# Performance work log

Hardware: AMD Instinct MI355X
Metric: run time of the kernel (lower is better)

## Reference

```python
import jax, jax.numpy as jnp
import numpy as np

NUM_ENTS = 100000
NUM_RELS2 = 1000  # num_rels * 2
H_DIM = 128
NUM_EDGES = 2000000
RRELU_SLOPE = (1.0 / 8.0 + 1.0 / 3.0) / 2.0  # F.rrelu eval-mode negative slope


def l2_normalize(x, eps=1e-12):
    # F.normalize along last dim
    n = jnp.sqrt(jnp.sum(x * x, axis=-1, keepdims=True))
    return x / jnp.maximum(n, eps)


def setup_inputs() -> dict:
    key = jax.random.key(0)
    ks = jax.random.split(key, 11)
    s = 1.0 / np.sqrt(H_DIM)
    return {
        "ent_emb": jax.random.normal(ks[0], (NUM_ENTS, H_DIM), jnp.float32),
        "rel_emb": jax.random.normal(ks[1], (NUM_RELS2, H_DIM), jnp.float32) * s,
        "his": jax.random.normal(ks[2], (NUM_ENTS, H_DIM), jnp.float32),
        "W_neighbor": jax.random.normal(ks[3], (H_DIM, H_DIM), jnp.float32) * s,
        "W_self": jax.random.normal(ks[4], (H_DIM, H_DIM), jnp.float32) * s,
        "time_gate_weight": jax.random.normal(ks[5], (H_DIM, H_DIM), jnp.float32) * s,
        "time_gate_bias": jnp.zeros((H_DIM,), jnp.float32),
        "edge_norm": jax.random.uniform(ks[6], (NUM_EDGES,), jnp.float32),
        "src": jax.random.randint(ks[7], (NUM_EDGES,), 0, NUM_ENTS, jnp.int32),
        "dst": jax.random.randint(ks[8], (NUM_EDGES,), 0, NUM_ENTS, jnp.int32),
        "etype": jax.random.randint(ks[9], (NUM_EDGES,), 0, NUM_RELS2, jnp.int32),
    }


def reference(ent_emb, rel_emb, his, W_neighbor, W_self, time_gate_weight,
              time_gate_bias, edge_norm, src, dst, etype):
    # layer_norm=True branch: L2-normalize entity embeddings (F.normalize)
    h = l2_normalize(ent_emb)                                   # [N, D]
    # UnionRGCNLayer message: (h[src] + rel_emb[etype]) @ W, scaled by edge norm
    node = h[src] + rel_emb[etype]                              # [E, D] gather
    msg = (node @ W_neighbor) * edge_norm[:, None]              # [E, D]
    agg = jax.ops.segment_sum(msg, dst, num_segments=NUM_ENTS)  # [N, D] scatter
    # self-loop + rrelu (eval mode: leaky with mean slope)
    h_cur = agg + h @ W_self
    h_cur = jnp.where(h_cur >= 0, h_cur, RRELU_SLOPE * h_cur)
    # time gate: blend current with historical embedding
    gate = jax.nn.sigmoid(h_cur @ time_gate_weight + time_gate_bias)
    out = gate * h_cur + (1.0 - gate) * his
    return out
```

## Files before the change

### kernel.cpp

```cpp
#include <hip/hip_runtime.h>
#include <math.h>

#define NUM_ENTS   100000
#define HD         128
#define NUM_EDGES  2000000
#define NUM_RELS2  1000
#define RRELU_SLOPE 0.22916666666666666f
#define NBLK 391
#define NPAD (NBLK * 256)
#define EQ4  (NUM_EDGES / 4)
#define EBLK ((EQ4 + 255) / 256)

#define SB_CNT 391
#define SB_HB  25000
#define SB_RB  125
#define SB_WP  24
#define SB_TOTAL (SB_CNT + SB_HB + SB_RB + SB_WP)

typedef __attribute__((ext_vector_type(8))) short bf16x8;
typedef __attribute__((ext_vector_type(4))) float f32x4;

__device__ __forceinline__ float bf2f(unsigned short h) {
    union { unsigned int u; float f; } v;
    v.u = ((unsigned int)h) << 16;
    return v.f;
}
__device__ __forceinline__ void unpack2(unsigned int u, float& lo, float& hi) {
    union { unsigned int u; float f; } a, b;
    a.u = u << 16;
    b.u = u & 0xffff0000u;
    lo = a.f; hi = b.f;
}
__device__ __forceinline__ unsigned short f2bf(float f) {
    union { float f; unsigned int u; } v; v.f = f;
    unsigned int r = 0x7fffu + ((v.u >> 16) & 1u);
    return (unsigned short)((v.u + r) >> 16);
}

__global__ void __launch_bounds__(256)
setup_kernel(const float* __restrict__ ent, const float* __restrict__ rel,
             const float* __restrict__ Wn, const float* __restrict__ Ws,
             const float* __restrict__ Wt,
             int* __restrict__ cnt, unsigned short* __restrict__ hb,
             unsigned short* __restrict__ rb, unsigned short* __restrict__ Wp) {
    const int bid = blockIdx.x, tid = threadIdx.x;
    if (bid < SB_CNT) {
        cnt[bid * 256 + tid] = 0;
    } else if (bid < SB_CNT + SB_HB) {
        const int row = (bid - SB_CNT) * 4 + (tid >> 6);
        const int lane = tid & 63;
        const float2 v = *(const float2*)(ent + (size_t)row * HD + lane * 2);
        float ss = v.x * v.x + v.y * v.y;
        #pragma unroll
        for (int m = 1; m < 64; m <<= 1) ss += __shfl_xor(ss, m, 64);
        const float inv = 1.0f / fmaxf(sqrtf(ss), 1e-12f);
        const unsigned int o = (unsigned int)f2bf(v.x * inv) |
                               ((unsigned int)f2bf(v.y * inv) << 16);
        *(unsigned int*)(hb + (size_t)row * HD + lane * 2) = o;
    } else if (bid < SB_CNT + SB_HB + SB_RB) {
        const int i = (bid - SB_CNT - SB_HB) * 256 + tid;
        const float4 v = ((const float4*)rel)[i];
        ushort4 o;
        o.x = f2bf(v.x); o.y = f2bf(v.y); o.z = f2bf(v.z); o.w = f2bf(v.w);
        ((ushort4*)rb)[i] = o;
    } else {
        const int blk = (bid - SB_CNT - SB_HB - SB_RB) * 4 + (tid >> 6);
        const int lane = tid & 63;
        const int w = blk >> 5, rem = blk & 31, t = rem >> 2, kt = rem & 3;
        const float* W = (w == 0) ? Wn : (w == 1) ? Ws : Wt;
        const int n  = t * 16 + (lane & 15);
        const int k0 = kt * 32 + (lane >> 4) * 8;
        unsigned short tmp[8];
        #pragma unroll
        for (int j = 0; j < 8; ++j) tmp[j] = f2bf(W[(size_t)(k0 + j) * HD + n]);
        unsigned short* d = Wp + ((size_t)blk * 64 + lane) * 8;
        *(ushort4*)(d + 0) = make_ushort4(tmp[0], tmp[1], tmp[2], tmp[3]);
        *(ushort4*)(d + 4) = make_ushort4(tmp[4], tmp[5], tmp[6], tmp[7]);
    }
}

__global__ void __launch_bounds__(256)
hist_kernel(const int* __restrict__ dst, int* __restrict__ cnt, int* __restrict__ pos) {
    const int i = blockIdx.x * 256 + threadIdx.x;
    if (i < EQ4) {
        const int4 d4 = ((const int4*)dst)[i];
        int4 p4;
        p4.x = atomicAdd(&cnt[d4.x], 1);
        p4.y = atomicAdd(&cnt[d4.y], 1);
        p4.z = atomicAdd(&cnt[d4.z], 1);
        p4.w = atomicAdd(&cnt[d4.w], 1);
        ((int4*)pos)[i] = p4;
    }
}

__global__ void __launch_bounds__(256)
scan1_kernel(const int* __restrict__ cnt, int* __restrict__ offs, int* __restrict__ bsum) {
    __shared__ int tmp[256];
    const int t = threadIdx.x;
    const int i = blockIdx.x * 256 + t;
    const int v = cnt[i];
    tmp[t] = v;
    __syncthreads();
    #pragma unroll
    for (int d = 1; d < 256; d <<= 1) {
        const int a = (t >= d) ? tmp[t - d] : 0;
        __syncthreads();
        tmp[t] += a;
        __syncthreads();
    }
    offs[i] = tmp[t] - v;
    if (t == 255) bsum[blockIdx.x] = tmp[255];
}

__global__ void __launch_bounds__(512)
scan2_kernel(int* __restrict__ bsum) {
    __shared__ int tmp[512];
    const int t = threadIdx.x;
    const int v = (t < NBLK) ? bsum[t] : 0;
    tmp[t] = v;
    __syncthreads();
    #pragma unroll
    for (int d = 1; d < 512; d <<= 1) {
        const int a = (t >= d) ? tmp[t - d] : 0;
        __syncthreads();
        tmp[t] += a;
        __syncthreads();
    }
    if (t < NBLK) bsum[t] = tmp[t] - v;
}

__global__ void __launch_bounds__(256)
scan3_kernel(int* __restrict__ offs, const int* __restrict__ bsum) {
    const int i = blockIdx.x * 256 + threadIdx.x;
    offs[i] += bsum[blockIdx.x];
}

__global__ void __launch_bounds__(256)
permute_kernel(const int* __restrict__ dst, const int* __restrict__ src,
               const int* __restrict__ ety, const float* __restrict__ enorm,
               const int* __restrict__ offs, const int* __restrict__ pos,
               uint2* __restrict__ recs) {
    const int i = blockIdx.x * 256 + threadIdx.x;
    if (i < EQ4) {
        const int4 d4 = ((const int4*)dst)[i];
        const int4 s4 = ((const int4*)src)[i];
        const int4 t4 = ((const int4*)ety)[i];
        const float4 n4 = ((const float4*)enorm)[i];
        const int4 p4 = ((const int4*)pos)[i];
        recs[offs[d4.x] + p4.x] = make_uint2((unsigned int)s4.x | ((unsigned int)t4.x << 17), __float_as_uint(n4.x));
        recs[offs[d4.y] + p4.y] = make_uint2((unsigned int)s4.y | ((unsigned int)t4.y << 17), __float_as_uint(n4.y));
        recs[offs[d4.z] + p4.z] = make_uint2((unsigned int)s4.z | ((unsigned int)t4.z << 17), __float_as_uint(n4.z));
        recs[offs[d4.w] + p4.w] = make_uint2((unsigned int)s4.w | ((unsigned int)t4.w << 17), __float_as_uint(n4.w));
    }
}

__device__ __forceinline__ void accum8(float* acc, uint4 hv, uint4 rv, float w) {
    float h0, h1, r0, r1;
    unpack2(hv.x, h0, h1); unpack2(rv.x, r0, r1);
    acc[0] += (h0 + r0) * w; acc[1] += (h1 + r1) * w;
    unpack2(hv.y, h0, h1); unpack2(rv.y, r0, r1);
    acc[2] += (h0 + r0) * w; acc[3] += (h1 + r1) * w;
    unpack2(hv.z, h0, h1); unpack2(rv.z, r0, r1);
    acc[4] += (h0 + r0) * w; acc[5] += (h1 + r1) * w;
    unpack2(hv.w, h0, h1); unpack2(rv.w, r0, r1);
    acc[6] += (h0 + r0) * w; acc[7] += (h1 + r1) * w;
}

__global__ void __launch_bounds__(256, 4)
gather_mfma(const unsigned short* __restrict__ hb,
            const unsigned short* __restrict__ rb,
            const int* __restrict__ offs,
            const uint2* __restrict__ recs,
            const unsigned short* __restrict__ Wp,
            const float* __restrict__ bias,
            const float* __restrict__ his,
            float* __restrict__ out) {
    __shared__ unsigned short tile[4][16 * 136];
    const int tid = threadIdx.x;
    const int wv = tid >> 6, lane = tid & 63;
    const int m0 = blockIdx.x * 64 + wv * 16;
    if (m0 >= NUM_ENTS) return;
    const int grp = lane >> 4, sub = lane & 15;
    const int rA = lane & 15, quad = lane >> 4;
    unsigned short* T = tile[wv];
    const unsigned short* hbp = hb + sub * 8;
    const unsigned short* rbp = rb + sub * 8;

    #pragma unroll
    for (int b = 0; b < 4; ++b) {
        const int rloc = b * 4 + grp;
        const int d = m0 + rloc;
        const int beg = offs[d], end = offs[d + 1];
        float acc[8] = {0.f, 0.f, 0.f, 0.f, 0.f, 0.f, 0.f, 0.f};
        int i = beg;
        uint2 rcA[4];
        #pragma unroll
        for (int k = 0; k < 4; ++k) rcA[k] = recs[min(i + k, NUM_EDGES - 1)];
        while (__any(i < end)) {
            uint2 rcB[4];
            #pragma unroll
            for (int k = 0; k < 4; ++k) rcB[k] = recs[min(i + 4 + k, NUM_EDGES - 1)];
            uint4 hv[4], rv[4]; float w[4];
            #pragma unroll
            for (int k = 0; k < 4; ++k) {
                w[k] = (i + k) < end ? __uint_as_float(rcA[k].y) : 0.f;
                hv[k] = *(const uint4*)(hbp + (size_t)(rcA[k].x & 0x1FFFFu) * HD);
                rv[k] = *(const uint4*)(rbp + (size_t)(rcA[k].x >> 17) * HD);
            }
            #pragma unroll
            for (int k = 0; k < 4; ++k) accum8(acc, hv[k], rv[k], w[k]);
            #pragma unroll
            for (int k = 0; k < 4; ++k) rcA[k] = rcB[k];
            i += 4;
        }
        unsigned short* dT = T + rloc * 136 + sub * 8;
        *(ushort4*)(dT + 0) = make_ushort4(f2bf(acc[0]), f2bf(acc[1]), f2bf(acc[2]), f2bf(acc[3]));
        *(ushort4*)(dT + 4) = make_ushort4(f2bf(acc[4]), f2bf(acc[5]), f2bf(acc[6]), f2bf(acc[7]));
    }

    const bf16x8* WF = (const bf16x8*)Wp;
    f32x4 acc1[8];
    #pragma unroll
    for (int t = 0; t < 8; ++t) acc1[t] = (f32x4)0.f;

    #pragma unroll
    for (int ph = 0; ph < 2; ++ph) {
        bf16x8 a[4];
        if (ph == 0) {
            #pragma unroll
            for (int kt = 0; kt < 4; ++kt)
                a[kt] = *(const bf16x8*)(T + rA * 136 + kt * 32 + quad * 8);
        } else {
            const unsigned short* base = hb + (size_t)(m0 + rA) * HD + quad * 8;
            #pragma unroll
            for (int kt = 0; kt < 4; ++kt)
                a[kt] = *(const bf16x8*)(base + kt * 32);
        }
        #pragma unroll
        for (int t = 0; t < 8; ++t) {
            #pragma unroll
            for (int kt = 0; kt < 4; ++kt) {
                const bf16x8 bfr = WF[(size_t)(ph * 32 + t * 4 + kt) * 64 + lane];
                acc1[t] = __builtin_amdgcn_mfma_f32_16x16x32_bf16(a[kt], bfr, acc1[t], 0, 0, 0);
            }
        }
    }

    #pragma unroll
    for (int t = 0; t < 8; ++t)
        #pragma unroll
        for (int r = 0; r < 4; ++r)
            acc1[t][r] = acc1[t][r] >= 0.f ? acc1[t][r] : RRELU_SLOPE * acc1[t][r];

    #pragma unroll
    for (int t = 0; t < 8; ++t)
        #pragma unroll
        for (int r = 0; r < 4; ++r)
            T[(quad * 4 + r) * 136 + t * 16 + rA] = f2bf(acc1[t][r]);

    bf16x8 a3[4];
    #pragma unroll
    for (int kt = 0; kt < 4; ++kt)
        a3[kt] = *(const bf16x8*)(T + rA * 136 + kt * 32 + quad * 8);

    #pragma unroll
    for (int t = 0; t < 8; ++t) {
        const float bn = bias[t * 16 + rA];
        f32x4 c2 = (f32x4){bn, bn, bn, bn};
        #pragma unroll
        for (int kt = 0; kt < 4; ++kt) {
            const bf16x8 bfr = WF[(size_t)(64 + t * 4 + kt) * 64 + lane];
            c2 = __builtin_amdgcn_mfma_f32_16x16x32_bf16(a3[kt], bfr, c2, 0, 0, 0);
        }
        const int col = t * 16 + rA;
        #pragma unroll
        for (int r = 0; r < 4; ++r) {
            const size_t row = (size_t)(m0 + quad * 4 + r);
            const float g = 1.f / (1.f + __expf(-c2[r]));
            const float h = his[row * HD + col];
            out[row * HD + col] = g * acc1[t][r] + (1.f - g) * h;
        }
    }
}

extern "C" void kernel_launch(void* const* d_in, const int* in_sizes, int n_in,
                              void* d_out, int out_size, void* d_ws, size_t ws_size,
                              hipStream_t stream) {
    const float* ent   = (const float*)d_in[0];
    const float* rel   = (const float*)d_in[1];
    const float* his   = (const float*)d_in[2];
    const float* Wn    = (const float*)d_in[3];
    const float* Ws    = (const float*)d_in[4];
    const float* Wt    = (const float*)d_in[5];
    const float* bias  = (const float*)d_in[6];
    const float* enorm = (const float*)d_in[7];
    const int* src = (const int*)d_in[8];
    const int* dst = (const int*)d_in[9];
    const int* ety = (const int*)d_in[10];
    float* out = (float*)d_out;

    char* p = (char*)d_ws;
    unsigned short* hb = (unsigned short*)p;  p += (size_t)NUM_ENTS * HD * 2;
    unsigned short* rb = (unsigned short*)p;  p += (size_t)NUM_RELS2 * HD * 2;
    unsigned short* Wp = (unsigned short*)p;  p += (size_t)96 * 64 * 8 * 2;
    int* cnt  = (int*)p;                      p += (size_t)NPAD * 4;
    int* offs = (int*)p;                      p += (size_t)NPAD * 4;
    int* bsum = (int*)p;                      p += 512 * 4;
    int* pos  = (int*)p;                      p += (size_t)NUM_EDGES * 4;
    uint2* recs = (uint2*)p;

    setup_kernel<<<SB_TOTAL, 256, 0, stream>>>(ent, rel, Wn, Ws, Wt, cnt, hb, rb, Wp);
    hist_kernel<<<EBLK, 256, 0, stream>>>(dst, cnt, pos);
    scan1_kernel<<<NBLK, 256, 0, stream>>>(cnt, offs, bsum);
    scan2_kernel<<<1, 512, 0, stream>>>(bsum);
    scan3_kernel<<<NBLK, 256, 0, stream>>>(offs, bsum);
    permute_kernel<<<EBLK, 256, 0, stream>>>(dst, src, ety, enorm, offs, pos, recs);
    gather_mfma<<<(NUM_ENTS + 63) / 64, 256, 0, stream>>>(hb, rb, offs, recs, Wp, bias, his, out);
}
```

Measured before the change: 433.0 us.

## Split gather block work across waves: 16 rows per block, waves share MFMA columns

Each block now handles 16 destination rows instead of 64. All 256 threads gather one row each per 16-lane group, into one shared tile. The MFMA output columns are then split across the four waves, two 16-column tiles each, with block barriers between the stages. This quadruples the grid and cuts per-thread gather serialization and accumulator registers, which should improve latency hiding. The cost is three __syncthreads per block and redundant A-fragment loads in each wave.

New measurement: 423.2 us. 1.02x faster.

```diff
diff --git a/kernel.cpp b/kernel.cpp
--- a/kernel.cpp
+++ b/kernel.cpp
@@ -175,21 +175,17 @@
             const float* __restrict__ bias,
             const float* __restrict__ his,
             float* __restrict__ out) {
-    __shared__ unsigned short tile[4][16 * 136];
+    __shared__ unsigned short T[16 * 136];
     const int tid = threadIdx.x;
+    const int m0 = blockIdx.x * 16;
+    const int grp = tid >> 4, sub = tid & 15;
     const int wv = tid >> 6, lane = tid & 63;
-    const int m0 = blockIdx.x * 64 + wv * 16;
-    if (m0 >= NUM_ENTS) return;
-    const int grp = lane >> 4, sub = lane & 15;
     const int rA = lane & 15, quad = lane >> 4;
-    unsigned short* T = tile[wv];
     const unsigned short* hbp = hb + sub * 8;
     const unsigned short* rbp = rb + sub * 8;
 
-    #pragma unroll
-    for (int b = 0; b < 4; ++b) {
-        const int rloc = b * 4 + grp;
-        const int d = m0 + rloc;
+    {
+        const int d = m0 + grp;
         const int beg = offs[d], end = offs[d + 1];
         float acc[8] = {0.f, 0.f, 0.f, 0.f, 0.f, 0.f, 0.f, 0.f};
         int i = beg;
@@ -213,50 +209,56 @@
             for (int k = 0; k < 4; ++k) rcA[k] = rcB[k];
             i += 4;
         }
-        unsigned short* dT = T + rloc * 136 + sub * 8;
+        unsigned short* dT = T + grp * 136 + sub * 8;
         *(ushort4*)(dT + 0) = make_ushort4(f2bf(acc[0]), f2bf(acc[1]), f2bf(acc[2]), f2bf(acc[3]));
         *(ushort4*)(dT + 4) = make_ushort4(f2bf(acc[4]), f2bf(acc[5]), f2bf(acc[6]), f2bf(acc[7]));
     }
+    __syncthreads();
 
     const bf16x8* WF = (const bf16x8*)Wp;
-    f32x4 acc1[8];
-    #pragma unroll
-    for (int t = 0; t < 8; ++t) acc1[t] = (f32x4)0.f;
-
-    #pragma unroll
-    for (int ph = 0; ph < 2; ++ph) {
-        bf16x8 a[4];
-        if (ph == 0) {
-            #pragma unroll
-            for (int kt = 0; kt < 4; ++kt)
-                a[kt] = *(const bf16x8*)(T + rA * 136 + kt * 32 + quad * 8);
-        } else {
-            const unsigned short* base = hb + (size_t)(m0 + rA) * HD + quad * 8;
-            #pragma unroll
-            for (int kt = 0; kt < 4; ++kt)
-                a[kt] = *(const bf16x8*)(base + kt * 32);
-        }
-        #pragma unroll
-        for (int t = 0; t < 8; ++t) {
-            #pragma unroll
-            for (int kt = 0; kt < 4; ++kt) {
-                const bf16x8 bfr = WF[(size_t)(ph * 32 + t * 4 + kt) * 64 + lane];
-                acc1[t] = __builtin_amdgcn_mfma_f32_16x16x32_bf16(a[kt], bfr, acc1[t], 0, 0, 0);
-            }
-        }
-    }
-
-    #pragma unroll
-    for (int t = 0; t < 8; ++t)
+    bf16x8 a1[4], a2[4];
+    #pragma unroll
+    for (int kt = 0; kt < 4; ++kt)
+        a1[kt] = *(const bf16x8*)(T + rA * 136 + kt * 32 + quad * 8);
+    {
+        const unsigned short* base = hb + (size_t)(m0 + rA) * HD + quad * 8;
+        #pragma unroll
+        for (int kt = 0; kt < 4; ++kt)
+            a2[kt] = *(const bf16x8*)(base + kt * 32);
+    }
+
+    f32x4 acc1[2];
+    #pragma unroll
+    for (int tt = 0; tt < 2; ++tt) acc1[tt] = (f32x4)0.f;
+
+    #pragma unroll
+    for (int tt = 0; tt < 2; ++tt) {
+        const int t = wv * 2 + tt;
+        #pragma unroll
+        for (int kt = 0; kt < 4; ++kt) {
+            const bf16x8 bfr = WF[(size_t)(t * 4 + kt) * 64 + lane];
+            acc1[tt] = __builtin_amdgcn_mfma_f32_16x16x32_bf16(a1[kt], bfr, acc1[tt], 0, 0, 0);
+        }
+        #pragma unroll
+        for (int kt = 0; kt < 4; ++kt) {
+            const bf16x8 bfr = WF[(size_t)(32 + t * 4 + kt) * 64 + lane];
+            acc1[tt] = __builtin_amdgcn_mfma_f32_16x16x32_bf16(a2[kt], bfr, acc1[tt], 0, 0, 0);
+        }
+    }
+
+    #pragma unroll
+    for (int tt = 0; tt < 2; ++tt)
         #pragma unroll
         for (int r = 0; r < 4; ++r)
-            acc1[t][r] = acc1[t][r] >= 0.f ? acc1[t][r] : RRELU_SLOPE * acc1[t][r];
-
-    #pragma unroll
-    for (int t = 0; t < 8; ++t)
+            acc1[tt][r] = acc1[tt][r] >= 0.f ? acc1[tt][r] : RRELU_SLOPE * acc1[tt][r];
+
+    __syncthreads();
+    #pragma unroll
+    for (int tt = 0; tt < 2; ++tt)
         #pragma unroll
         for (int r = 0; r < 4; ++r)
-            T[(quad * 4 + r) * 136 + t * 16 + rA] = f2bf(acc1[t][r]);
+            T[(quad * 4 + r) * 136 + (wv * 2 + tt) * 16 + rA] = f2bf(acc1[tt][r]);
+    __syncthreads();
 
     bf16x8 a3[4];
     #pragma unroll
@@ -264,7 +266,8 @@
         a3[kt] = *(const bf16x8*)(T + rA * 136 + kt * 32 + quad * 8);
 
     #pragma unroll
-    for (int t = 0; t < 8; ++t) {
+    for (int tt = 0; tt < 2; ++tt) {
+        const int t = wv * 2 + tt;
         const float bn = bias[t * 16 + rA];
         f32x4 c2 = (f32x4){bn, bn, bn, bn};
         #pragma unroll
@@ -278,7 +281,7 @@
             const size_t row = (size_t)(m0 + quad * 4 + r);
             const float g = 1.f / (1.f + __expf(-c2[r]));
             const float h = his[row * HD + col];
-            out[row * HD + col] = g * acc1[t][r] + (1.f - g) * h;
+            out[row * HD + col] = g * acc1[tt][r] + (1.f - g) * h;
         }
     }
 }
@@ -315,5 +318,5 @@
     scan2_kernel<<<1, 512, 0, stream>>>(bsum);
     scan3_kernel<<<NBLK, 256, 0, stream>>>(offs, bsum);
     permute_kernel<<<EBLK, 256, 0, stream>>>(dst, src, ety, enorm, offs, pos, recs);
-    gather_mfma<<<(NUM_ENTS + 63) / 64, 256, 0, stream>>>(hb, rb, offs, recs, Wp, bias, his, out);
-}
+    gather_mfma<<<NUM_ENTS / 16, 256, 0, stream>>>(hb, rb, offs, recs, Wp, bias, his, out);
+}
```
